# Kernel optimization log

Hardware: AMD Instinct MI355X
Metric: run time of the kernel (lower is better)

The kernel has to match this reference:

```python
import jax, jax.numpy as jnp
import numpy as np


def setup_inputs() -> dict:
    key = jax.random.key(0)
    k1, k2, k3, k4 = jax.random.split(key, 4)
    B, S, D = 16, 1024, 300      # batch, set_size, word_vector_dim
    K = 64                        # hidden_set_size == compressed_dim (element_dim)
    O = 256                       # set_representation_dim (output_dim)
    Xs = jax.random.normal(k1, (B, S, D), dtype=jnp.float32)
    # Linear(word_vector_dim -> hidden_set_size)
    W = jax.random.normal(k2, (K, D), dtype=jnp.float32) * (1.0 / np.sqrt(D))
    b = jax.random.normal(k3, (K,), dtype=jnp.float32) * 0.01
    # hidden_sets: (output_dim, hidden_set_size, element_dim) with xavier-normal scale
    xav = np.sqrt(2.0 / (K + K))
    hidden_sets = jax.random.normal(k4, (O, K, K), dtype=jnp.float32) * xav
    return {"Xs": Xs, "W": W, "b": b, "hidden_sets": hidden_sets}


def reference(Xs, W, b, hidden_sets):
    # compress: [B,S,D] @ [D,K] + b -> [B,S,K]
    Xc = jnp.einsum('bsd,kd->bsk', Xs, W) + b
    # bipartite_match: tensordot over element_dim -> [B,S,O,N] (N = hidden_set_size)
    G = jax.nn.relu(jnp.einsum('bsk,onk->bson', Xc, hidden_sets))
    # set_size (1024) > hidden_set_size (64): max over hidden-set axis, sum over set axis
    value = jnp.sum(jnp.max(G, axis=-1), axis=1)  # [B,O]
    return value
```

## Files before the change

### kernel.cpp

```cpp
#include <hip/hip_runtime.h>
#include <hip/hip_bf16.h>

#define B_  16
#define S_  1024
#define D_  300
#define K_  64
#define O_  256
#define M_  (B_*S_)

#define LROW 80

typedef __attribute__((ext_vector_type(8)))  short s8b;
typedef __attribute__((ext_vector_type(4)))  float f32x4;
typedef __attribute__((ext_vector_type(16))) float f32x16;

#define MFMA16(a,b,c) __builtin_amdgcn_mfma_f32_16x16x32_bf16((a),(b),(c),0,0,0)
#define MFMA32(a,b,c) __builtin_amdgcn_mfma_f32_32x32x16_bf16((a),(b),(c),0,0,0)

__device__ __forceinline__ unsigned short bf16_bits(float f) {
    return __builtin_bit_cast(unsigned short, __float2bfloat16(f));
}

__device__ __forceinline__ s8b pack8(float4 f0, float4 f1) {
    union { unsigned short us[8]; s8b v; } pk;
    pk.us[0]=bf16_bits(f0.x); pk.us[1]=bf16_bits(f0.y);
    pk.us[2]=bf16_bits(f0.z); pk.us[3]=bf16_bits(f0.w);
    pk.us[4]=bf16_bits(f1.x); pk.us[5]=bf16_bits(f1.y);
    pk.us[6]=bf16_bits(f1.z); pk.us[7]=bf16_bits(f1.w);
    return pk.v;
}

#define C_BLK 1024
#define H_BLK 512

__global__ __launch_bounds__(256) void k_head(
        const float* __restrict__ Xs,
        const float* __restrict__ W,
        const float* __restrict__ bias,
        const float* __restrict__ H,
        __hip_bfloat16* __restrict__ Xc,
        __hip_bfloat16* __restrict__ Hb,
        float* __restrict__ out) {
    int bx = blockIdx.x, tid = threadIdx.x;
    if (bx >= C_BLK) {
        if (bx < C_BLK + H_BLK) {
            int g = ((bx - C_BLK) * 256 + tid) * 8;
            float4 f0 = *(const float4*)(H + g);
            float4 f1 = *(const float4*)(H + g + 4);
            *(uint4*)(Hb + g) = __builtin_bit_cast(uint4, pack8(f0, f1));
        } else {
            float4 z = {0.f,0.f,0.f,0.f};
            float4* o4 = (float4*)out;
#pragma unroll
            for (int i = 0; i < 4; ++i) o4[tid * 4 + i] = z;
        }
        return;
    }

    int w    = tid >> 6, lane = tid & 63;
    int q    = lane >> 4, r = lane & 15;
    int row0 = bx * 16;
    int col0 = w * 16;

    f32x4 acc0 = {0.f,0.f,0.f,0.f}, acc1 = {0.f,0.f,0.f,0.f};
    const float* arow = Xs + (size_t)(row0 + r) * D_;
    const float* brow = W  + (size_t)(col0 + r) * D_;
    const float4 z4 = {0.f,0.f,0.f,0.f};

#pragma unroll
    for (int ks = 0; ks < 10; ++ks) {
        int k0 = ks * 32 + q * 8;
        float4 a0 = (k0     < D_) ? *(const float4*)(arow + k0)     : z4;
        float4 a1 = (k0 + 4 < D_) ? *(const float4*)(arow + k0 + 4) : z4;
        float4 b0 = (k0     < D_) ? *(const float4*)(brow + k0)     : z4;
        float4 b1 = (k0 + 4 < D_) ? *(const float4*)(brow + k0 + 4) : z4;
        s8b av = pack8(a0, a1);
        s8b bv = pack8(b0, b1);
        if (ks & 1) acc1 = MFMA16(av, bv, acc1);
        else        acc0 = MFMA16(av, bv, acc0);
    }
#pragma unroll
    for (int i = 0; i < 4; ++i) {
        int orow = row0 + q * 4 + i;
        int c    = col0 + r;
        Xc[(size_t)orow * K_ + c] =
            __float2bfloat16(acc0[i] + acc1[i] + bias[c]);
    }
}

__global__ __launch_bounds__(512, 4) void k_fused(
        const __hip_bfloat16* __restrict__ Xc,
        const __hip_bfloat16* __restrict__ Hb,
        float* __restrict__ out) {
    __shared__ __hip_bfloat16 lx[2][64 * LROW];
    int tid   = threadIdx.x;
    int w     = tid >> 6, lane = tid & 63;
    int half  = lane >> 5, l31 = lane & 31;
    int bx    = blockIdx.x;
    int batch = bx >> 6;
    int oq    = (bx >> 1) & 31;
    int sh    = bx & 1;
    int o     = oq * 8 + w;

    s8b af[2][4];
#pragma unroll
    for (int nt = 0; nt < 2; ++nt) {
        const __hip_bfloat16* hrow =
            Hb + (size_t)(o * 64 + nt * 32 + l31) * 64 + half * 8;
#pragma unroll
        for (int ks = 0; ks < 4; ++ks)
            af[nt][ks] = __builtin_bit_cast(s8b, *(const uint4*)(hrow + ks * 16));
    }

    const __hip_bfloat16* xbase =
        Xc + ((size_t)batch * S_ + (size_t)sh * 512) * K_;

    int sr = tid >> 3, sc = tid & 7;

    {
        uint4 v = *(const uint4*)(xbase + (size_t)sr * K_ + sc * 8);
        *(uint4*)(&lx[0][sr * LROW + sc * 8]) = v;
    }
    __syncthreads();

    float total = 0.0f;
    for (int s = 0; s < 8; ++s) {
        uint4 npf;
        if (s < 7) {
            const __hip_bfloat16* nsrc = xbase + (size_t)(s + 1) * 64 * K_;
            npf = *(const uint4*)(nsrc + (size_t)sr * K_ + sc * 8);
        }
        const __hip_bfloat16* buf = lx[s & 1];
#pragma unroll
        for (int t = 0; t < 2; ++t) {
            int rr = t * 32 + l31;
            s8b bf[4];
#pragma unroll
            for (int ks = 0; ks < 4; ++ks)
                bf[ks] = __builtin_bit_cast(s8b,
                    *(const uint4*)(&buf[rr * LROW + (2 * ks + half) * 8]));

            f32x16 a0 = {0.f,0.f,0.f,0.f,0.f,0.f,0.f,0.f,
                         0.f,0.f,0.f,0.f,0.f,0.f,0.f,0.f};
            f32x16 a1 = a0;
#pragma unroll
            for (int ks = 0; ks < 4; ++ks) {
                a0 = MFMA32(af[0][ks], bf[ks], a0);
                a1 = MFMA32(af[1][ks], bf[ks], a1);
            }
            float m0 = fmaxf(fmaxf(a0[0], a0[1]), a0[2]);
            m0 = fmaxf(fmaxf(m0, a0[3]), a0[4]);
            m0 = fmaxf(fmaxf(m0, a0[5]), a0[6]);
            m0 = fmaxf(m0, a0[7]);
            float m1 = fmaxf(fmaxf(a0[8], a0[9]), a0[10]);
            m1 = fmaxf(fmaxf(m1, a0[11]), a0[12]);
            m1 = fmaxf(fmaxf(m1, a0[13]), a0[14]);
            m1 = fmaxf(m1, a0[15]);
            float m2 = fmaxf(fmaxf(a1[0], a1[1]), a1[2]);
            m2 = fmaxf(fmaxf(m2, a1[3]), a1[4]);
            m2 = fmaxf(fmaxf(m2, a1[5]), a1[6]);
            m2 = fmaxf(m2, a1[7]);
            float m3 = fmaxf(fmaxf(a1[8], a1[9]), a1[10]);
            m3 = fmaxf(fmaxf(m3, a1[11]), a1[12]);
            m3 = fmaxf(fmaxf(m3, a1[13]), a1[14]);
            m3 = fmaxf(m3, a1[15]);
            float v = fmaxf(fmaxf(fmaxf(m0, m1), fmaxf(m2, m3)), 0.0f);
            v = fmaxf(v, __shfl_xor(v, 32));
            total += v;
        }
        if (s < 7) {
            *(uint4*)(&lx[(s + 1) & 1][sr * LROW + sc * 8]) = npf;
            __syncthreads();
        }
    }
    total += __shfl_xor(total, 1);
    total += __shfl_xor(total, 2);
    total += __shfl_xor(total, 4);
    total += __shfl_xor(total, 8);
    total += __shfl_xor(total, 16);
    if (lane == 0) atomicAdd(out + batch * O_ + o, total);
}

extern "C" void kernel_launch(void* const* d_in, const int* in_sizes, int n_in,
                              void* d_out, int out_size, void* d_ws, size_t ws_size,
                              hipStream_t stream) {
    const float* Xs   = (const float*)d_in[0];
    const float* W    = (const float*)d_in[1];
    const float* bias = (const float*)d_in[2];
    const float* H    = (const float*)d_in[3];
    float* out = (float*)d_out;

    char* ws = (char*)d_ws;
    __hip_bfloat16* Hb = (__hip_bfloat16*)(ws);
    __hip_bfloat16* Xc = (__hip_bfloat16*)(ws + 2097152);

    k_head <<<C_BLK + H_BLK + 1, 256, 0, stream>>>(Xs, W, bias, H, Xc, Hb, out);
    k_fused<<<B_ * (O_ / 8) * 2, 512, 0, stream>>>(Xc, Hb, out);
}
```

Before: 108.6 us.

## Stream Xc tiles to LDS with direct global-to-LDS loads in a 4-stage pipeline

The fused kernel now loads Xc tiles straight into LDS with global_load_lds instead of staging them through registers. It keeps four LDS buffers with three loads in flight, using explicit vmcnt waits and barriers per stage. The padded row layout is replaced by an XOR swizzle of the 16-byte columns to avoid bank conflicts, and MFMA sections get raised wave priority. This targets global-load latency and register-staging overhead, at the cost of fragile hand-written wait counts and more LDS per block, which may reduce occupancy.

```diff
diff --git a/kernel.cpp b/kernel.cpp
--- a/kernel.cpp
+++ b/kernel.cpp
@@ -8,14 +8,17 @@
 #define O_  256
 #define M_  (B_*S_)
 
-#define LROW 80
-
 typedef __attribute__((ext_vector_type(8)))  short s8b;
 typedef __attribute__((ext_vector_type(4)))  float f32x4;
 typedef __attribute__((ext_vector_type(16))) float f32x16;
 
 #define MFMA16(a,b,c) __builtin_amdgcn_mfma_f32_16x16x32_bf16((a),(b),(c),0,0,0)
 #define MFMA32(a,b,c) __builtin_amdgcn_mfma_f32_32x32x16_bf16((a),(b),(c),0,0,0)
+
+typedef __attribute__((address_space(1))) const void gas_void;
+typedef __attribute__((address_space(3))) void las_void;
+#define GLOAD16(g, l) __builtin_amdgcn_global_load_lds( \
+    (gas_void*)(g), (las_void*)(l), 16, 0, 0)
 
 __device__ __forceinline__ unsigned short bf16_bits(float f) {
     return __builtin_bit_cast(unsigned short, __float2bfloat16(f));
@@ -28,6 +31,26 @@
     pk.us[4]=bf16_bits(f1.x); pk.us[5]=bf16_bits(f1.y);
     pk.us[6]=bf16_bits(f1.z); pk.us[7]=bf16_bits(f1.w);
     return pk.v;
+}
+
+__device__ __forceinline__ float maxreduce32(const f32x16& a0, const f32x16& a1) {
+    float m0 = fmaxf(fmaxf(a0[0], a0[1]), a0[2]);
+    m0 = fmaxf(fmaxf(m0, a0[3]), a0[4]);
+    m0 = fmaxf(fmaxf(m0, a0[5]), a0[6]);
+    m0 = fmaxf(m0, a0[7]);
+    float m1 = fmaxf(fmaxf(a0[8], a0[9]), a0[10]);
+    m1 = fmaxf(fmaxf(m1, a0[11]), a0[12]);
+    m1 = fmaxf(fmaxf(m1, a0[13]), a0[14]);
+    m1 = fmaxf(m1, a0[15]);
+    float m2 = fmaxf(fmaxf(a1[0], a1[1]), a1[2]);
+    m2 = fmaxf(fmaxf(m2, a1[3]), a1[4]);
+    m2 = fmaxf(fmaxf(m2, a1[5]), a1[6]);
+    m2 = fmaxf(m2, a1[7]);
+    float m3 = fmaxf(fmaxf(a1[8], a1[9]), a1[10]);
+    m3 = fmaxf(fmaxf(m3, a1[11]), a1[12]);
+    m3 = fmaxf(fmaxf(m3, a1[13]), a1[14]);
+    m3 = fmaxf(m3, a1[15]);
+    return fmaxf(fmaxf(fmaxf(m0, m1), fmaxf(m2, m3)), 0.0f);
 }
 
 #define C_BLK 1024
@@ -92,10 +115,11 @@
         const __hip_bfloat16* __restrict__ Xc,
         const __hip_bfloat16* __restrict__ Hb,
         float* __restrict__ out) {
-    __shared__ __hip_bfloat16 lx[2][64 * LROW];
+    __shared__ __hip_bfloat16 lx[4][64 * 64];
     int tid   = threadIdx.x;
     int w     = tid >> 6, lane = tid & 63;
     int half  = lane >> 5, l31 = lane & 31;
+    int xm    = l31 & 7;
     int bx    = blockIdx.x;
     int batch = bx >> 6;
     int oq    = (bx >> 1) & 31;
@@ -111,26 +135,33 @@
         for (int ks = 0; ks < 4; ++ks)
             af[nt][ks] = __builtin_bit_cast(s8b, *(const uint4*)(hrow + ks * 16));
     }
+    asm volatile("s_waitcnt vmcnt(0)" ::: "memory");
 
     const __hip_bfloat16* xbase =
         Xc + ((size_t)batch * S_ + (size_t)sh * 512) * K_;
 
-    int sr = tid >> 3, sc = tid & 7;
-
-    {
-        uint4 v = *(const uint4*)(xbase + (size_t)sr * K_ + sc * 8);
-        *(uint4*)(&lx[0][sr * LROW + sc * 8]) = v;
-    }
-    __syncthreads();
+    const __hip_bfloat16* gs =
+        xbase + (size_t)(8 * w + (lane >> 3)) * K_
+              + (((lane & 7) ^ (lane >> 3)) * 8);
+
+#pragma unroll
+    for (int p = 0; p < 3; ++p)
+        GLOAD16(gs + (size_t)p * 64 * K_, &lx[p][w * 512]);
 
     float total = 0.0f;
+#pragma unroll
     for (int s = 0; s < 8; ++s) {
-        uint4 npf;
-        if (s < 7) {
-            const __hip_bfloat16* nsrc = xbase + (size_t)(s + 1) * 64 * K_;
-            npf = *(const uint4*)(nsrc + (size_t)sr * K_ + sc * 8);
-        }
-        const __hip_bfloat16* buf = lx[s & 1];
+        if      (s <= 5) asm volatile("s_waitcnt vmcnt(2)" ::: "memory");
+        else if (s == 6) asm volatile("s_waitcnt vmcnt(1)" ::: "memory");
+        else             asm volatile("s_waitcnt vmcnt(0)" ::: "memory");
+        __builtin_amdgcn_s_barrier();
+        asm volatile("" ::: "memory");
+        __builtin_amdgcn_sched_barrier(0);
+
+        if (s < 5)
+            GLOAD16(gs + (size_t)(s + 3) * 64 * K_, &lx[(s + 3) & 3][w * 512]);
+
+        const __hip_bfloat16* buf = lx[s & 3];
 #pragma unroll
         for (int t = 0; t < 2; ++t) {
             int rr = t * 32 + l31;
@@ -138,39 +169,22 @@
 #pragma unroll
             for (int ks = 0; ks < 4; ++ks)
                 bf[ks] = __builtin_bit_cast(s8b,
-                    *(const uint4*)(&buf[rr * LROW + (2 * ks + half) * 8]));
+                    *(const uint4*)(&buf[rr * K_ + (((2 * ks + half) ^ xm) * 8)]));
 
             f32x16 a0 = {0.f,0.f,0.f,0.f,0.f,0.f,0.f,0.f,
                          0.f,0.f,0.f,0.f,0.f,0.f,0.f,0.f};
             f32x16 a1 = a0;
+            __builtin_amdgcn_s_setprio(1);
 #pragma unroll
             for (int ks = 0; ks < 4; ++ks) {
                 a0 = MFMA32(af[0][ks], bf[ks], a0);
                 a1 = MFMA32(af[1][ks], bf[ks], a1);
             }
-            float m0 = fmaxf(fmaxf(a0[0], a0[1]), a0[2]);
-            m0 = fmaxf(fmaxf(m0, a0[3]), a0[4]);
-            m0 = fmaxf(fmaxf(m0, a0[5]), a0[6]);
-            m0 = fmaxf(m0, a0[7]);
-            float m1 = fmaxf(fmaxf(a0[8], a0[9]), a0[10]);
-            m1 = fmaxf(fmaxf(m1, a0[11]), a0[12]);
-            m1 = fmaxf(fmaxf(m1, a0[13]), a0[14]);
-            m1 = fmaxf(m1, a0[15]);
-            float m2 = fmaxf(fmaxf(a1[0], a1[1]), a1[2]);
-            m2 = fmaxf(fmaxf(m2, a1[3]), a1[4]);
-            m2 = fmaxf(fmaxf(m2, a1[5]), a1[6]);
-            m2 = fmaxf(m2, a1[7]);
-            float m3 = fmaxf(fmaxf(a1[8], a1[9]), a1[10]);
-            m3 = fmaxf(fmaxf(m3, a1[11]), a1[12]);
-            m3 = fmaxf(fmaxf(m3, a1[13]), a1[14]);
-            m3 = fmaxf(m3, a1[15]);
-            float v = fmaxf(fmaxf(fmaxf(m0, m1), fmaxf(m2, m3)), 0.0f);
+            __builtin_amdgcn_s_setprio(0);
+
+            float v = maxreduce32(a0, a1);
             v = fmaxf(v, __shfl_xor(v, 32));
             total += v;
-        }
-        if (s < 7) {
-            *(uint4*)(&lx[(s + 1) & 1][sr * LROW + sc * 8]) = npf;
-            __syncthreads();
         }
     }
     total += __shfl_xor(total, 1);
```

Result: no change. 109.8 us (+1.2%).
